# Kernel optimization log

Hardware: AMD Instinct MI355X
Metric: run time of the kernel (lower is better)

The kernel has to match this reference:

```python
import jax, jax.numpy as jnp
import numpy as np

N, C, H, W = 8, 512, 56, 56
CI = 256  # inter_channels = in_channels // reduction


def setup_inputs() -> dict:
    key = jax.random.key(0)
    ks = jax.random.split(key, 9)
    std = 0.01
    return {
        "x": jax.random.normal(ks[0], (N, C, H, W), dtype=jnp.float32),
        "W_g": jax.random.normal(ks[1], (CI, C), dtype=jnp.float32) * std,
        "b_g": jnp.zeros((CI,), dtype=jnp.float32),
        "W_theta": jax.random.normal(ks[2], (CI, C), dtype=jnp.float32) * std,
        "b_theta": jnp.zeros((CI,), dtype=jnp.float32),
        "W_phi": jax.random.normal(ks[3], (CI, C), dtype=jnp.float32) * std,
        "b_phi": jnp.zeros((CI,), dtype=jnp.float32),
        "W_out": jax.random.normal(ks[4], (C, CI), dtype=jnp.float32) * std,
        "b_out": jax.random.normal(ks[5], (C,), dtype=jnp.float32) * std,
    }


def _proj(Wt, b, xf):
    # 1x1 conv == channel GEMM over flattened spatial positions: (n, o, L)
    return jnp.einsum('oc,ncl->nol', Wt, xf) + b[None, :, None]


def reference(x, W_g, b_g, W_theta, b_theta, W_phi, b_phi, W_out, b_out):
    n, c, h, w = x.shape
    L = h * w
    xf = x.reshape(n, c, L)

    g_x = _proj(W_g, b_g, xf).transpose(0, 2, 1)          # (n, L, ci)
    theta_x = _proj(W_theta, b_theta, xf).transpose(0, 2, 1)  # (n, L, ci)
    phi_x = _proj(W_phi, b_phi, xf)                        # (n, ci, L)

    ci = theta_x.shape[-1]
    # embedded_gaussian with use_scale=True
    pairwise = jnp.einsum('nqc,nck->nqk', theta_x, phi_x) / jnp.sqrt(
        jnp.asarray(ci, dtype=x.dtype))
    pairwise = jax.nn.softmax(pairwise, axis=-1)           # (n, L, L)

    y = jnp.einsum('nqk,nkc->nqc', pairwise, g_x)          # (n, L, ci)
    y = y.transpose(0, 2, 1)                               # (n, ci, L)
    out = _proj(W_out, b_out, y).reshape(n, c, h, w)
    return x + out
```

## Files before the change

kernel.cpp:

```cpp
#include <hip/hip_runtime.h>
#include <stdint.h>

#define NB 8
#define CC 512
#define LL 3136
#define CIN 256

typedef __attribute__((ext_vector_type(8))) short bf8;
typedef __attribute__((ext_vector_type(4))) float f4;
typedef __attribute__((ext_vector_type(16))) float f16v;
typedef __attribute__((ext_vector_type(4))) int i4;

__device__ __forceinline__ f4 mfma_bf16(bf8 a, bf8 b, f4 c) {
  return __builtin_amdgcn_mfma_f32_16x16x32_bf16(a, b, c, 0, 0, 0);
}

__device__ __forceinline__ f16v mfma32(bf8 a, bf8 b, f16v c) {
  return __builtin_amdgcn_mfma_f32_32x32x16_bf16(a, b, c, 0, 0, 0);
}

__device__ __forceinline__ unsigned short f2bf(float f) {
  unsigned int u = __float_as_uint(f);
  u += 0x7FFFu + ((u >> 16) & 1u);
  return (unsigned short)(u >> 16);
}

__device__ __forceinline__ int cvtpk_bf16(float lo, float hi) {
  int r;
  asm("v_cvt_pk_bf16_f32 %0, %1, %2" : "=v"(r) : "v"(lo), "v"(hi));
  return r;
}

__device__ __forceinline__ void gload_lds16(const unsigned short* g, unsigned short* l) {
  __builtin_amdgcn_global_load_lds(
      (const __attribute__((address_space(1))) void*)g,
      (__attribute__((address_space(3))) void*)l, 16, 0, 0);
}

__global__ void k_convw(const float* Wth, const float* Wph, const float* Wg, const float* Wout,
                        unsigned short* dst) {
  int i = blockIdx.x * 256 + threadIdx.x;
  int which = i >> 17;
  int off = i & 131071;
  const float* s = which == 0 ? Wth : which == 1 ? Wph : which == 2 ? Wg : Wout;
  dst[i] = f2bf(s[off]);
}

__global__ __launch_bounds__(256) void k_xT(const float* x, unsigned short* xT) {
  __shared__ unsigned short tile[64][66];
  const int lt = blockIdx.x, n = blockIdx.y, ct = blockIdx.z;
  const int t = threadIdx.x;
  const float* xb = x + (size_t)n * CC * LL + (size_t)(ct * 64) * LL + lt * 64;
  const int tl = t & 63, trow = t >> 6;
#pragma unroll
  for (int i = 0; i < 16; ++i) {
    int c = i * 4 + trow;
    tile[c][tl] = f2bf(xb[(size_t)c * LL + tl]);
  }
  __syncthreads();
  unsigned short* xo = xT + (size_t)n * LL * CC + (size_t)(lt * 64) * CC + ct * 64;
  const int tc = t & 63, lrow = t >> 6;
#pragma unroll
  for (int i = 0; i < 16; ++i) {
    int l = i * 4 + lrow;
    xo[(size_t)l * CC + tc] = tile[tc][l];
  }
}

__global__ __launch_bounds__(256, 2) void k_proj(const unsigned short* Wbf,
    const float* bth, const float* bph, const float* bg,
    const unsigned short* xT, unsigned short* QT, unsigned short* KT, unsigned short* Vb) {
  __shared__ unsigned short wtile[2][8192];
  __shared__ unsigned short xtile[2][8192];
  const int bid = blockIdx.x;
  const int n = bid & 7, t = bid >> 3;
  const int lt = t % 25, z = t / 25;
  const int proj = z >> 1, cith = z & 1;
  const int tid = threadIdx.x;
  const int wave = tid >> 6, lane = tid & 63;
  const int quad = lane >> 4, c16 = lane & 15;

  const unsigned short* Wg = Wbf + proj * 131072 + (size_t)(cith * 128) * CC;
  const unsigned short* Xg = xT + (size_t)n * LL * CC + (size_t)(lt * 128) * CC;

  auto issue = [&](int chunk, int b) {
    const int cb = chunk * 64;
#pragma unroll
    for (int i = 0; i < 4; ++i) {
      int seg = i * 4 + wave;
      int p = seg * 64 + lane;
      int r = p >> 3, sl = p & 7, g = sl ^ (r & 7);
      gload_lds16(Wg + (size_t)r * CC + cb + g * 8, &wtile[b][seg * 512]);
    }
#pragma unroll
    for (int i = 0; i < 4; ++i) {
      int seg = i * 4 + wave;
      int p = seg * 64 + lane;
      int r = p >> 3, sl = p & 7, g = sl ^ (r & 7);
      gload_lds16(Xg + (size_t)r * CC + cb + g * 8, &xtile[b][seg * 512]);
    }
  };

  const f4 zz = {0.f, 0.f, 0.f, 0.f};
  f4 acc[2][8];
#pragma unroll
  for (int i = 0; i < 2; ++i)
#pragma unroll
    for (int j = 0; j < 8; ++j) acc[i][j] = zz;

  issue(0, 0);
  for (int chunk = 0; chunk < 8; ++chunk) {
    __syncthreads();
    if (chunk + 1 < 8) issue(chunk + 1, (chunk + 1) & 1);
    const int bb = chunk & 1;
#pragma unroll
    for (int kc = 0; kc < 2; ++kc) {
      const int slot = (kc * 4 + quad) ^ (c16 & 7);
      bf8 wf[2], xf[8];
#pragma unroll
      for (int sub = 0; sub < 2; ++sub)
        wf[sub] = *(const bf8*)(&wtile[bb][(wave * 32 + sub * 16 + c16) * 64 + slot * 8]);
#pragma unroll
      for (int nt = 0; nt < 8; ++nt)
        xf[nt] = *(const bf8*)(&xtile[bb][(nt * 16 + c16) * 64 + slot * 8]);
      if (proj < 2) {
#pragma unroll
        for (int sub = 0; sub < 2; ++sub)
#pragma unroll
          for (int nt = 0; nt < 8; ++nt)
            acc[sub][nt] = mfma_bf16(wf[sub], xf[nt], acc[sub][nt]);
      } else {
#pragma unroll
        for (int sub = 0; sub < 2; ++sub)
#pragma unroll
          for (int nt = 0; nt < 8; ++nt)
            acc[sub][nt] = mfma_bf16(xf[nt], wf[sub], acc[sub][nt]);
      }
    }
  }

  if (proj < 2) {
    const float* bias = proj == 0 ? bth : bph;
    unsigned short* dst = proj == 0 ? QT : KT;
#pragma unroll
    for (int sub = 0; sub < 2; ++sub) {
      const int ciB = cith * 128 + wave * 32 + sub * 16 + quad * 4;
      const float b0 = bias[ciB + 0], b1 = bias[ciB + 1];
      const float b2 = bias[ciB + 2], b3 = bias[ciB + 3];
#pragma unroll
      for (int nt = 0; nt < 8; ++nt) {
        int l = lt * 128 + nt * 16 + c16;
        if (l < LL) {
          ushort4 v;
          v.x = f2bf(acc[sub][nt][0] + b0);
          v.y = f2bf(acc[sub][nt][1] + b1);
          v.z = f2bf(acc[sub][nt][2] + b2);
          v.w = f2bf(acc[sub][nt][3] + b3);
          *(ushort4*)(dst + ((size_t)n * LL + l) * CIN + ciB) = v;
        }
      }
    }
  } else {
#pragma unroll
    for (int sub = 0; sub < 2; ++sub) {
      const int ci = cith * 128 + wave * 32 + sub * 16 + c16;
      const float bv = bg[ci];
#pragma unroll
      for (int nt = 0; nt < 8; ++nt) {
        int l = lt * 128 + nt * 16 + quad * 4;
        if (l < LL) {
          ushort4 v;
          v.x = f2bf(acc[sub][nt][0] + bv);
          v.y = f2bf(acc[sub][nt][1] + bv);
          v.z = f2bf(acc[sub][nt][2] + bv);
          v.w = f2bf(acc[sub][nt][3] + bv);
          *(ushort4*)(Vb + ((size_t)n * CIN + ci) * LL + l) = v;
        }
      }
    }
  }
}

__global__ __launch_bounds__(256, 2) void k_attn(const unsigned short* QT, const unsigned short* KT,
                                                 const unsigned short* Vb, unsigned short* Opart,
                                                 float* denp) {
  __shared__ unsigned short kbuf[2][8192];
  __shared__ unsigned short vbuf[2][8192];
  const int bid = blockIdx.x;
  const int n = bid & 7, ks = (bid >> 3) & 1, qb = bid >> 4;
  const int tid = threadIdx.x;
  const int wave = tid >> 6, lane = tid & 63;
  const int l31 = lane & 31, half = lane >> 5;
  int q0 = qb * 128 + wave * 32;
  const bool do_store = q0 < LL;
  if (q0 > LL - 32) q0 = LL - 32;
  const unsigned short* Qb = QT + ((size_t)n * LL + q0) * CIN;
  const unsigned short* Kks = KT + (size_t)n * LL * CIN + (size_t)(ks * 49 * 32) * CIN;
  const unsigned short* Vks = Vb + (size_t)n * CIN * LL + ks * 49 * 32;

  const float qs = 0.09016844005556021f;
  bf8 qf[16];
#pragma unroll
  for (int kc = 0; kc < 16; ++kc) {
    bf8 q = *(const bf8*)(Qb + (size_t)l31 * CIN + kc * 16 + half * 8);
#pragma unroll
    for (int e = 0; e < 8; ++e) {
      float f = __uint_as_float(((unsigned)(unsigned short)q[e]) << 16) * qs;
      q[e] = (short)f2bf(f);
    }
    qf[kc] = q;
  }

  f16v o[8];
#pragma unroll
  for (int t = 0; t < 8; ++t)
#pragma unroll
    for (int r = 0; r < 16; ++r) o[t][r] = 0.f;
  float sden = 0.f;

  auto issue = [&](int kt, int b) {
    const int k0 = kt * 32;
    const unsigned short* Kg = Kks + (size_t)k0 * CIN;
    const unsigned short* Vg = Vks + k0;
#pragma unroll
    for (int i = 0; i < 4; ++i) {
      int seg = i * 4 + wave;
      int idx = seg * 64 + lane;
      {
        int r = idx >> 5, sl = idx & 31, g = sl ^ r;
        gload_lds16(Kg + r * CIN + g * 8, &kbuf[b][seg * 512]);
      }
      {
        int r = idx >> 2, sl = idx & 3, g = sl ^ ((r >> 1) & 3);
        gload_lds16(Vg + (size_t)r * LL + g * 8, &vbuf[b][seg * 512]);
      }
    }
  };

  issue(0, 0);
  for (int kt = 0; kt < 49; ++kt) {
    __syncthreads();
    if (kt + 1 < 49) issue(kt + 1, (kt + 1) & 1);
    const int b = kt & 1;
    const unsigned short* kb = &kbuf[b][0];
    const unsigned short* vbp = &vbuf[b][0];

    f16v sc;
#pragma unroll
    for (int r = 0; r < 16; ++r) sc[r] = 0.f;
    __builtin_amdgcn_s_setprio(1);
#pragma unroll
    for (int kc = 0; kc < 16; ++kc) {
      int slot = (kc * 2 + half) ^ l31;
      bf8 kf = *(const bf8*)(kb + l31 * 256 + slot * 8);
      sc = mfma32(kf, qf[kc], sc);
    }
    __builtin_amdgcn_s_setprio(0);

    bf8 af[2];
#pragma unroll
    for (int m = 0; m < 2; ++m) {
      float p0 = __builtin_amdgcn_exp2f(sc[8 * m + 0]);
      float p1 = __builtin_amdgcn_exp2f(sc[8 * m + 1]);
      float p2 = __builtin_amdgcn_exp2f(sc[8 * m + 2]);
      float p3 = __builtin_amdgcn_exp2f(sc[8 * m + 3]);
      float p4 = __builtin_amdgcn_exp2f(sc[8 * m + 4]);
      float p5 = __builtin_amdgcn_exp2f(sc[8 * m + 5]);
      float p6 = __builtin_amdgcn_exp2f(sc[8 * m + 6]);
      float p7 = __builtin_amdgcn_exp2f(sc[8 * m + 7]);
      sden += ((p0 + p1) + (p2 + p3)) + ((p4 + p5) + (p6 + p7));
      int x0 = cvtpk_bf16(p0, p1);
      int y0 = cvtpk_bf16(p4, p5);
      int x1 = cvtpk_bf16(p2, p3);
      int y1 = cvtpk_bf16(p6, p7);
      asm("v_permlane32_swap_b32 %0, %1" : "+v"(x0), "+v"(y0));
      asm("v_permlane32_swap_b32 %0, %1" : "+v"(x1), "+v"(y1));
      i4 w;
      w[0] = x0; w[1] = x1; w[2] = y0; w[3] = y1;
      af[m] = *(bf8*)&w;
    }

    __builtin_amdgcn_s_setprio(1);
#pragma unroll
    for (int t = 0; t < 8; ++t) {
#pragma unroll
      for (int kc2 = 0; kc2 < 2; ++kc2) {
        int slot = (kc2 * 2 + half) ^ ((l31 >> 1) & 3);
        bf8 v = *(const bf8*)(vbp + (t * 32 + l31) * 32 + slot * 8);
        o[t] = mfma32(af[kc2], v, o[t]);
      }
    }
    __builtin_amdgcn_s_setprio(0);
  }

  sden += __shfl_xor(sden, 32);

  if (do_store) {
    if (lane < 32) denp[((size_t)ks * NB + n) * LL + q0 + l31] = sden;
    unsigned short* Ob = Opart + (((size_t)ks * NB + n) * LL + q0) * CIN;
#pragma unroll
    for (int t = 0; t < 8; ++t)
#pragma unroll
      for (int r = 0; r < 16; ++r) {
        int row = (r & 3) + 8 * (r >> 2) + 4 * half;
        Ob[(size_t)row * CIN + t * 32 + l31] = f2bf(o[t][r]);
      }
  }
}

__global__ void k_den(const float* denp, float* invden) {
  int i = blockIdx.x * 256 + threadIdx.x;
  if (i < NB * LL) invden[i] = 1.f / (denp[i] + denp[NB * LL + i]);
}

__global__ __launch_bounds__(256, 2) void k_out(const unsigned short* O0, const unsigned short* O1,
    const unsigned short* Wo, const float* bout, const float* invden,
    const float* x, float* out) {
  __shared__ unsigned short wtile[2][8192];
  __shared__ unsigned short otile[2][8192];
  const int bid = blockIdx.x;
  const int n = bid & 7, t = bid >> 3;
  const int lt = t % 25, cth = t / 25;
  const int tid = threadIdx.x;
  const int wave = tid >> 6, lane = tid & 63;
  const int quad = lane >> 4, c16 = lane & 15;

  const unsigned short* Wg = Wo + (size_t)(cth * 128) * CIN;
  const unsigned short* Og0 = O0 + ((size_t)n * LL + lt * 128) * CIN;
  const unsigned short* Og1 = O1 + ((size_t)n * LL + lt * 128) * CIN;

  auto issue = [&](int chunk, int b) {
    const int cb = (chunk & 3) * 64;
    const unsigned short* Og = chunk < 4 ? Og0 : Og1;
#pragma unroll
    for (int i = 0; i < 4; ++i) {
      int seg = i * 4 + wave;
      int p = seg * 64 + lane;
      int r = p >> 3, sl = p & 7, g = sl ^ (r & 7);
      gload_lds16(Wg + (size_t)r * CIN + cb + g * 8, &wtile[b][seg * 512]);
    }
#pragma unroll
    for (int i = 0; i < 4; ++i) {
      int seg = i * 4 + wave;
      int p = seg * 64 + lane;
      int r = p >> 3, sl = p & 7, g = sl ^ (r & 7);
      gload_lds16(Og + (size_t)r * CIN + cb + g * 8, &otile[b][seg * 512]);
    }
  };

  const f4 zz = {0.f, 0.f, 0.f, 0.f};
  f4 acc[8][2];
#pragma unroll
  for (int i = 0; i < 8; ++i)
#pragma unroll
    for (int j = 0; j < 2; ++j) acc[i][j] = zz;

  issue(0, 0);
  for (int chunk = 0; chunk < 8; ++chunk) {
    __syncthreads();
    if (chunk + 1 < 8) issue(chunk + 1, (chunk + 1) & 1);
    const int bb = chunk & 1;
#pragma unroll
    for (int kc = 0; kc < 2; ++kc) {
      const int slot = (kc * 4 + quad) ^ (c16 & 7);
      bf8 wf[2], ofr[8];
#pragma unroll
      for (int sub = 0; sub < 2; ++sub)
        wf[sub] = *(const bf8*)(&wtile[bb][(wave * 32 + sub * 16 + c16) * 64 + slot * 8]);
#pragma unroll
      for (int nt = 0; nt < 8; ++nt)
        ofr[nt] = *(const bf8*)(&otile[bb][(nt * 16 + c16) * 64 + slot * 8]);
#pragma unroll
      for (int nt = 0; nt < 8; ++nt)
#pragma unroll
        for (int sub = 0; sub < 2; ++sub)
          acc[nt][sub] = mfma_bf16(ofr[nt], wf[sub], acc[nt][sub]);
    }
  }

#pragma unroll
  for (int sub = 0; sub < 2; ++sub) {
    const int c = cth * 128 + wave * 32 + sub * 16 + c16;
    const float bv = bout[c];
#pragma unroll
    for (int nt = 0; nt < 8; ++nt) {
      int l = lt * 128 + nt * 16 + quad * 4;
      if (l < LL) {
        f4 iv = *(const f4*)(invden + (size_t)n * LL + l);
        size_t base = ((size_t)n * CC + c) * LL + l;
        f4 xv = *(const f4*)(x + base);
        f4 r;
        r[0] = xv[0] + bv + acc[nt][sub][0] * iv[0];
        r[1] = xv[1] + bv + acc[nt][sub][1] * iv[1];
        r[2] = xv[2] + bv + acc[nt][sub][2] * iv[2];
        r[3] = xv[3] + bv + acc[nt][sub][3] * iv[3];
        *(f4*)(out + base) = r;
      }
    }
  }
}

extern "C" void kernel_launch(void* const* d_in, const int* in_sizes, int n_in,
                              void* d_out, int out_size, void* d_ws, size_t ws_size,
                              hipStream_t stream) {
  const float* x     = (const float*)d_in[0];
  const float* W_g   = (const float*)d_in[1];
  const float* b_g   = (const float*)d_in[2];
  const float* W_th  = (const float*)d_in[3];
  const float* b_th  = (const float*)d_in[4];
  const float* W_ph  = (const float*)d_in[5];
  const float* b_ph  = (const float*)d_in[6];
  const float* W_out = (const float*)d_in[7];
  const float* b_out = (const float*)d_in[8];

  char* ws = (char*)d_ws;
  const size_t SZ_W  = 1048576;
  const size_t SZ_P  = 12845056;
  unsigned short* Wbf = (unsigned short*)(ws);
  unsigned short* QT  = (unsigned short*)(ws + SZ_W);
  unsigned short* KT  = (unsigned short*)(ws + SZ_W + SZ_P);
  unsigned short* Vb  = (unsigned short*)(ws + SZ_W + 2 * SZ_P);
  unsigned short* xT  = (unsigned short*)(ws + SZ_W + 3 * SZ_P);
  unsigned short* O0  = xT;
  unsigned short* O1  = (unsigned short*)(ws + SZ_W + 4 * SZ_P);
  float* denp   = (float*)(ws + SZ_W + 5 * SZ_P);
  float* invden = (float*)(ws + SZ_W + 5 * SZ_P + 2 * NB * LL * 4);
  float* out = (float*)d_out;

  k_convw<<<2048, 256, 0, stream>>>(W_th, W_ph, W_g, W_out, Wbf);
  k_xT<<<dim3(49, 8, 8), 256, 0, stream>>>(x, xT);
  k_proj<<<1200, 256, 0, stream>>>(Wbf, b_th, b_ph, b_g, xT, QT, KT, Vb);
  k_attn<<<400, 256, 0, stream>>>(QT, KT, Vb, O0, denp);
  k_den<<<98, 256, 0, stream>>>(denp, invden);
  k_out<<<800, 256, 0, stream>>>(O0, O1, Wbf + 3 * 131072, b_out, invden, x, out);
}
```

Baseline: 290.5 us.

## Merge conversion kernels, fold denominator into output GEMM, vectorize transpose, raise MFMA priority

The weight conversion and the x transpose now run as one launch, and the separate reciprocal-denominator kernel is folded into k_out. k_out computes 1/den for its 128 columns into shared memory during the prologue. The transpose now uses float4 loads and ushort4 stores instead of scalar accesses. s_setprio is raised around the MFMA loops in k_proj and k_out. Together these cut two kernel launches and some memory traffic, at the cost of strided LDS reads in the transpose and a small extra prologue in k_out.

Result: faster. 279.3 us (-3.9%).

```diff
diff --git a/kernel.cpp b/kernel.cpp
--- a/kernel.cpp
+++ b/kernel.cpp
@@ -37,33 +37,47 @@
       (__attribute__((address_space(3))) void*)l, 16, 0, 0);
 }
 
-__global__ void k_convw(const float* Wth, const float* Wph, const float* Wg, const float* Wout,
-                        unsigned short* dst) {
-  int i = blockIdx.x * 256 + threadIdx.x;
-  int which = i >> 17;
-  int off = i & 131071;
-  const float* s = which == 0 ? Wth : which == 1 ? Wph : which == 2 ? Wg : Wout;
-  dst[i] = f2bf(s[off]);
-}
-
-__global__ __launch_bounds__(256) void k_xT(const float* x, unsigned short* xT) {
+__global__ __launch_bounds__(256) void k_cvt(const float* Wth, const float* Wph, const float* Wg,
+                                             const float* Wout, unsigned short* Wbf,
+                                             const float* x, unsigned short* xT) {
+  const int bid = blockIdx.x;
+  const int t = threadIdx.x;
+  if (bid >= 3136) {
+    int i = (bid - 3136) * 256 + t;
+    int which = i >> 17, off = i & 131071;
+    const float* s = which == 0 ? Wth : which == 1 ? Wph : which == 2 ? Wg : Wout;
+    Wbf[i] = f2bf(s[off]);
+    return;
+  }
   __shared__ unsigned short tile[64][66];
-  const int lt = blockIdx.x, n = blockIdx.y, ct = blockIdx.z;
-  const int t = threadIdx.x;
+  const int lt = bid % 49;
+  const int rest = bid / 49;
+  const int n = rest & 7, ct = rest >> 3;
   const float* xb = x + (size_t)n * CC * LL + (size_t)(ct * 64) * LL + lt * 64;
-  const int tl = t & 63, trow = t >> 6;
-#pragma unroll
-  for (int i = 0; i < 16; ++i) {
-    int c = i * 4 + trow;
-    tile[c][tl] = f2bf(xb[(size_t)c * LL + tl]);
+  {
+    const int lq = t & 15, cr = t >> 4;
+#pragma unroll
+    for (int p = 0; p < 4; ++p) {
+      int c = p * 16 + cr;
+      f4 v = *(const f4*)(xb + (size_t)c * LL + lq * 4);
+#pragma unroll
+      for (int j = 0; j < 4; ++j) tile[c][lq * 4 + j] = f2bf(v[j]);
+    }
   }
   __syncthreads();
   unsigned short* xo = xT + (size_t)n * LL * CC + (size_t)(lt * 64) * CC + ct * 64;
-  const int tc = t & 63, lrow = t >> 6;
-#pragma unroll
-  for (int i = 0; i < 16; ++i) {
-    int l = i * 4 + lrow;
-    xo[(size_t)l * CC + tc] = tile[tc][l];
+  {
+    const int cq = t & 15, lr = t >> 4;
+#pragma unroll
+    for (int p = 0; p < 4; ++p) {
+      int l = p * 16 + lr;
+      ushort4 s;
+      s.x = tile[cq * 4 + 0][l];
+      s.y = tile[cq * 4 + 1][l];
+      s.z = tile[cq * 4 + 2][l];
+      s.w = tile[cq * 4 + 3][l];
+      *(ushort4*)(xo + (size_t)l * CC + cq * 4) = s;
+    }
   }
 }
 
@@ -113,6 +127,7 @@
     __syncthreads();
     if (chunk + 1 < 8) issue(chunk + 1, (chunk + 1) & 1);
     const int bb = chunk & 1;
+    __builtin_amdgcn_s_setprio(1);
 #pragma unroll
     for (int kc = 0; kc < 2; ++kc) {
       const int slot = (kc * 4 + quad) ^ (c16 & 7);
@@ -137,6 +152,7 @@
             acc[sub][nt] = mfma_bf16(xf[nt], wf[sub], acc[sub][nt]);
       }
     }
+    __builtin_amdgcn_s_setprio(0);
   }
 
   if (proj < 2) {
@@ -308,16 +324,12 @@
   }
 }
 
-__global__ void k_den(const float* denp, float* invden) {
-  int i = blockIdx.x * 256 + threadIdx.x;
-  if (i < NB * LL) invden[i] = 1.f / (denp[i] + denp[NB * LL + i]);
-}
-
 __global__ __launch_bounds__(256, 2) void k_out(const unsigned short* O0, const unsigned short* O1,
-    const unsigned short* Wo, const float* bout, const float* invden,
+    const unsigned short* Wo, const float* bout, const float* denp,
     const float* x, float* out) {
   __shared__ unsigned short wtile[2][8192];
   __shared__ unsigned short otile[2][8192];
+  __shared__ float ivbuf[128];
   const int bid = blockIdx.x;
   const int n = bid & 7, t = bid >> 3;
   const int lt = t % 25, cth = t / 25;
@@ -356,10 +368,17 @@
     for (int j = 0; j < 2; ++j) acc[i][j] = zz;
 
   issue(0, 0);
+  if (tid < 128) {
+    int l = lt * 128 + tid;
+    float d = 1.f;
+    if (l < LL) d = 1.f / (denp[(size_t)n * LL + l] + denp[(size_t)(NB + n) * LL + l]);
+    ivbuf[tid] = d;
+  }
   for (int chunk = 0; chunk < 8; ++chunk) {
     __syncthreads();
     if (chunk + 1 < 8) issue(chunk + 1, (chunk + 1) & 1);
     const int bb = chunk & 1;
+    __builtin_amdgcn_s_setprio(1);
 #pragma unroll
     for (int kc = 0; kc < 2; ++kc) {
       const int slot = (kc * 4 + quad) ^ (c16 & 7);
@@ -376,6 +395,7 @@
         for (int sub = 0; sub < 2; ++sub)
           acc[nt][sub] = mfma_bf16(ofr[nt], wf[sub], acc[nt][sub]);
     }
+    __builtin_amdgcn_s_setprio(0);
   }
 
 #pragma unroll
@@ -386,7 +406,7 @@
     for (int nt = 0; nt < 8; ++nt) {
       int l = lt * 128 + nt * 16 + quad * 4;
       if (l < LL) {
-        f4 iv = *(const f4*)(invden + (size_t)n * LL + l);
+        f4 iv = *(const f4*)&ivbuf[nt * 16 + quad * 4];
         size_t base = ((size_t)n * CC + c) * LL + l;
         f4 xv = *(const f4*)(x + base);
         f4 r;
@@ -424,13 +444,10 @@
   unsigned short* O0  = xT;
   unsigned short* O1  = (unsigned short*)(ws + SZ_W + 4 * SZ_P);
   float* denp   = (float*)(ws + SZ_W + 5 * SZ_P);
-  float* invden = (float*)(ws + SZ_W + 5 * SZ_P + 2 * NB * LL * 4);
   float* out = (float*)d_out;
 
-  k_convw<<<2048, 256, 0, stream>>>(W_th, W_ph, W_g, W_out, Wbf);
-  k_xT<<<dim3(49, 8, 8), 256, 0, stream>>>(x, xT);
+  k_cvt<<<5184, 256, 0, stream>>>(W_th, W_ph, W_g, W_out, Wbf, x, xT);
   k_proj<<<1200, 256, 0, stream>>>(Wbf, b_th, b_ph, b_g, xT, QT, KT, Vb);
   k_attn<<<400, 256, 0, stream>>>(QT, KT, Vb, O0, denp);
-  k_den<<<98, 256, 0, stream>>>(denp, invden);
-  k_out<<<800, 256, 0, stream>>>(O0, O1, Wbf + 3 * 131072, b_out, invden, x, out);
-}
+  k_out<<<800, 256, 0, stream>>>(O0, O1, Wbf + 3 * 131072, b_out, denp, x, out);
+}
```
